# Performance work log

Measured on AMD Instinct MI355X. Metric: run time of the kernel, lower is better.

## Reference

```python
import jax, jax.numpy as jnp
import numpy as np

N = 100000      # nodes
E = 1600000     # edges
F_IN = 128      # num_features
H = 64          # hidden_channels
EPS = 1e-5      # batchnorm eps


def _bn(x, gamma, beta, mean, var):
    # inference-mode BatchNorm1d
    return (x - mean) * jax.lax.rsqrt(var + EPS) * gamma + beta


def setup_inputs() -> dict:
    key = jax.random.key(0)
    ks = jax.random.split(key, 16)

    def lin_w(k, fan_in, fan_out):
        return (jax.random.normal(k, (fan_in, fan_out), jnp.float32)
                * (1.0 / np.sqrt(fan_in)))

    return {
        "x": jax.random.normal(ks[0], (N, F_IN), jnp.float32),
        "edge_index": jax.random.randint(ks[1], (2, E), 0, N, dtype=jnp.int32),
        # node_encoder: Linear(F_IN,H) + BN
        "enc_W": lin_w(ks[2], F_IN, H), "enc_b": jnp.zeros((H,), jnp.float32),
        "enc_g": jnp.ones((H,), jnp.float32), "enc_beta": jnp.zeros((H,), jnp.float32),
        "enc_mean": jnp.zeros((H,), jnp.float32), "enc_var": jnp.ones((H,), jnp.float32),
        # GCNConv layers (PyG: lin without bias, bias added after aggregation)
        "conv1_W": lin_w(ks[3], H, H), "conv1_b": jnp.zeros((H,), jnp.float32),
        "conv2_W": lin_w(ks[4], H, H), "conv2_b": jnp.zeros((H,), jnp.float32),
        # edge_predictor: Linear(2H,H) + BN + Linear(H,1)
        "ep1_W": lin_w(ks[5], 2 * H, H), "ep1_b": jnp.zeros((H,), jnp.float32),
        "ep_g": jnp.ones((H,), jnp.float32), "ep_beta": jnp.zeros((H,), jnp.float32),
        "ep_mean": jnp.zeros((H,), jnp.float32), "ep_var": jnp.ones((H,), jnp.float32),
        "ep2_W": lin_w(ks[6], H, 1), "ep2_b": jnp.zeros((1,), jnp.float32),
    }


def reference(x, edge_index, enc_W, enc_b, enc_g, enc_beta, enc_mean, enc_var,
              conv1_W, conv1_b, conv2_W, conv2_b,
              ep1_W, ep1_b, ep_g, ep_beta, ep_mean, ep_var, ep2_W, ep2_b):
    row, col = edge_index[0], edge_index[1]

    # GCN normalization with added self-loops (symmetric D^-1/2 (A+I) D^-1/2)
    loops = jnp.arange(N, dtype=row.dtype)
    row_sl = jnp.concatenate([row, loops])          # [E+N]
    col_sl = jnp.concatenate([col, loops])
    deg = jax.ops.segment_sum(jnp.ones_like(col_sl, jnp.float32), col_sl, N)
    dinv = jnp.where(deg > 0, jax.lax.rsqrt(jnp.maximum(deg, 1.0)), 0.0)
    norm = dinv[row_sl] * dinv[col_sl]              # [E+N]

    def gcn_conv(h, W, b):
        hw = h @ W                                   # [N,H]
        msg = hw[row_sl] * norm[:, None]             # gather-scale  [E+N,H]
        return jax.ops.segment_sum(msg, col_sl, N) + b  # scatter-add

    # node encoder (inference: dropout = identity)
    h = jax.nn.relu(_bn(x @ enc_W + enc_b, enc_g, enc_beta, enc_mean, enc_var))
    h = jax.nn.relu(gcn_conv(h, conv1_W, conv1_b))
    h = jax.nn.relu(gcn_conv(h, conv2_W, conv2_b))
    node_embeddings = h

    # edge predictor: gather + cat + MLP + sigmoid
    ef = jnp.concatenate([h[row], h[col]], axis=1)   # [E, 2H]
    e = jax.nn.relu(_bn(ef @ ep1_W + ep1_b, ep_g, ep_beta, ep_mean, ep_var))
    edge_pred = jax.nn.sigmoid(e @ ep2_W + ep2_b)    # [E, 1]
    return node_embeddings, edge_pred
```

## Files before the change

### kernel.cpp

```cpp
#include <hip/hip_runtime.h>
#include <hip/hip_bf16.h>
#include <hip/hip_fp16.h>

#define NN 100000
#define NE 1600000
#define FIN 128
#define HD 64
#define NB_SCAN 391
#define NB_MF 1563
#define BSH 8
#define BUCK 256
#define NBUCK 392
#define BCAP 5120
#define CHUNK 4096
#define NCHUNK 391
#define ESPLIT 2
#define NEB (NBUCK*ESPLIT)
#define NFB 6250
#define NAGG 6250

typedef unsigned int uint32;
typedef _Float16 half8 __attribute__((ext_vector_type(8)));
typedef float f32x4 __attribute__((ext_vector_type(4)));
typedef float f32x8 __attribute__((ext_vector_type(8)));

__global__ void __launch_bounds__(256) k_part(const int* __restrict__ row,
                                              const int* __restrict__ col,
                                              int* __restrict__ bcnt,
                                              uint32* __restrict__ staged,
                                              uint32* __restrict__ posE){
    __shared__ int hist[NBUCK];
    __shared__ int base[NBUCK];
    int t = threadIdx.x;
    int e0 = blockIdx.x * CHUNK;
    int e1 = min(e0 + CHUNK, NE);
    for(int i = t; i < NBUCK; i += 256) hist[i] = 0;
    __syncthreads();
    for(int e = e0 + t; e < e1; e += 256)
        atomicAdd(&hist[col[e] >> BSH], 1);
    __syncthreads();
    for(int i = t; i < NBUCK; i += 256){
        int c = hist[i];
        base[i] = (c > 0) ? atomicAdd(&bcnt[i], c) : 0;
        hist[i] = 0;
    }
    __syncthreads();
    for(int e = e0 + t; e < e1; e += 256){
        int c = col[e], r = row[e];
        int b = c >> BSH;
        int pos = base[b] + atomicAdd(&hist[b], 1);
        if(pos < BCAP){
            staged[(size_t)b*BCAP + pos] = ((uint32)r << BSH) | (uint32)(c & (BUCK-1));
            posE[e] = (uint32)(b*BCAP + pos);
        } else posE[e] = 0xFFFFFFFFu;
    }
}

__global__ void __launch_bounds__(256) k_hist(const int* __restrict__ bcnt,
                                              const uint32* __restrict__ staged,
                                              int* __restrict__ deg){
    __shared__ int h[BUCK];
    int b = blockIdx.x, t = threadIdx.x;
    for(int i = t; i < BUCK; i += 256) h[i] = 0;
    __syncthreads();
    int cnt = min(bcnt[b], BCAP);
    const uint32* st = staged + (size_t)b*BCAP;
    for(int i = t; i < cnt; i += 256) atomicAdd(&h[st[i] & (BUCK-1)], 1);
    __syncthreads();
    for(int i = t; i < BUCK; i += 256){
        int n = b*BUCK + i;
        if(n < NN) deg[n] = h[i];
    }
}

__global__ void k_bsum(const int* __restrict__ deg, int* __restrict__ bsum){
    __shared__ int r[256];
    int t = threadIdx.x; int i = blockIdx.x*256 + t;
    r[t] = (i < NN) ? deg[i] : 0;
    __syncthreads();
    for(int off=128; off>0; off>>=1){ if(t<off) r[t]+=r[t+off]; __syncthreads(); }
    if(t==0) bsum[blockIdx.x] = r[0];
}

__global__ void k_top(int* __restrict__ bsum){
    __shared__ int s[512];
    int t = threadIdx.x;
    int v = (t < NB_SCAN) ? bsum[t] : 0;
    s[t] = v; __syncthreads();
    for(int off=1; off<512; off<<=1){
        int a = (t>=off)? s[t-off] : 0;
        __syncthreads();
        s[t] += a;
        __syncthreads();
    }
    if(t < NB_SCAN) bsum[t] = s[t] - v;
}

__global__ void k_scan(const int* __restrict__ deg, const int* __restrict__ bsum,
                       int* __restrict__ starts, float* __restrict__ dinv){
    __shared__ int s[256];
    int t = threadIdx.x; int i = blockIdx.x*256 + t;
    int d = (i<NN)? deg[i] : 0;
    s[t] = d; __syncthreads();
    for(int off=1; off<256; off<<=1){
        int a = (t>=off)? s[t-off] : 0;
        __syncthreads();
        s[t] += a;
        __syncthreads();
    }
    if(i < NN){
        starts[i] = bsum[blockIdx.x] + s[t] - d;
        dinv[i] = rsqrtf((float)(d + 1));
    }
}

__global__ void __launch_bounds__(256) k_fill2(const int* __restrict__ bcnt,
                                               const uint32* __restrict__ staged,
                                               const int* __restrict__ starts,
                                               int* __restrict__ csr){
    __shared__ int cur[BUCK];
    __shared__ int lcsr[BCAP];
    int b = blockIdx.x, t = threadIdx.x;
    int n0 = b*BUCK;
    int base = starts[min(n0, NN-1)];
    for(int i = t; i < BUCK; i += 256){
        int n = n0 + i;
        cur[i] = (n < NN) ? starts[n] - base : 0;
    }
    __syncthreads();
    int cnt = min(bcnt[b], BCAP);
    const uint32* st = staged + (size_t)b*BCAP;
    for(int i = t; i < cnt; i += 256){
        uint32 u = st[i];
        int p = atomicAdd(&cur[u & (BUCK-1)], 1);
        lcsr[p] = (int)(u >> BSH);
    }
    __syncthreads();
    for(int i = t; i < cnt; i += 256) csr[base + i] = lcsr[i];
}

__global__ void k_const(const float* __restrict__ encB, const float* __restrict__ encG,
                        const float* __restrict__ encBe, const float* __restrict__ encM,
                        const float* __restrict__ encV,
                        const float* __restrict__ ep1b, const float* __restrict__ epG,
                        const float* __restrict__ epBe, const float* __restrict__ epM,
                        const float* __restrict__ epV,
                        float* __restrict__ foldEnc, float* __restrict__ foldPre){
    int j = threadIdx.x;
    if(j < 64){
        float s = encG[j]*rsqrtf(encV[j]+1e-5f);
        foldEnc[j]      = s;
        foldEnc[64+j]   = (encB[j]-encM[j])*s + encBe[j];
        float sp = epG[j]*rsqrtf(epV[j]+1e-5f);
        foldPre[j]      = sp;
        foldPre[64+j]   = sp;
        foldPre[128+j]  = sp*(ep1b[j]-epM[j]) + epBe[j];
        foldPre[192+j]  = 0.f;
    }
}

__global__ void k_wprep(const float* __restrict__ encW, const float* __restrict__ c1W,
                        const float* __restrict__ c2W, const float* __restrict__ ep1W,
                        _Float16* __restrict__ wt){
    int i = blockIdx.x*256 + threadIdx.x;
    if(i < 8192){
        int n = i >> 7, k = i & 127;
        wt[i] = (_Float16)encW[k*64 + n];
    } else if(i < 12288){
        int j = i - 8192; int n = j >> 6, k = j & 63;
        wt[i] = (_Float16)c1W[k*64 + n];
    } else if(i < 16384){
        int j = i - 12288; int n = j >> 6, k = j & 63;
        wt[i] = (_Float16)c2W[k*64 + n];
    } else if(i < 24576){
        int j = i - 16384; int h = j >> 12; int jj = j & 4095;
        int n = jj >> 6, k = jj & 63;
        wt[i] = (_Float16)ep1W[(h*64 + k)*64 + n];
    }
}

template<int K, bool AF32, bool FOLD, bool RELU, bool SCALE, int OS>
__global__ void __launch_bounds__(256) k_mfma(const void* __restrict__ Ain,
                                              const _Float16* __restrict__ Bt,
                                              const float* __restrict__ fold,
                                              const float* __restrict__ rowscale,
                                              _Float16* __restrict__ outh){
    constexpr int PS = K + 8;
    __shared__ _Float16 As[64*PS];
    __shared__ _Float16 Bs[64*PS];
    int t = threadIdx.x;
    int m0 = blockIdx.x*64;
    int jh = blockIdx.y;
    {
        const _Float16* src = Bt + (size_t)jh*64*K;
        for(int idx = t; idx < 64*(K/8); idx += 256){
            int n = idx/(K/8), c = idx%(K/8);
            *(half8*)&Bs[n*PS + c*8] = *(const half8*)&src[n*K + c*8];
        }
    }
    if(AF32){
        const float* A = (const float*)Ain;
        for(int idx = t; idx < 64*(K/4); idx += 256){
            int r = idx/(K/4), c = idx%(K/4);
            int rowi = m0 + r; if(rowi >= NN) rowi = NN-1;
            float4 v = *(const float4*)&A[(size_t)rowi*K + c*4];
            _Float16* d = &As[r*PS + c*4];
            d[0]=(_Float16)v.x; d[1]=(_Float16)v.y; d[2]=(_Float16)v.z; d[3]=(_Float16)v.w;
        }
    } else {
        const _Float16* A = (const _Float16*)Ain;
        for(int idx = t; idx < 64*(K/8); idx += 256){
            int r = idx/(K/8), c = idx%(K/8);
            int rowi = m0 + r; if(rowi >= NN) rowi = NN-1;
            *(half8*)&As[r*PS + c*8] = *(const half8*)&A[(size_t)rowi*K + c*8];
        }
    }
    __syncthreads();
    int w = t>>6, l = t&63;
    int lm = l&15, q = l>>4;
    f32x4 acc0 = {0.f,0.f,0.f,0.f}, acc1 = {0.f,0.f,0.f,0.f};
    f32x4 acc2 = {0.f,0.f,0.f,0.f}, acc3 = {0.f,0.f,0.f,0.f};
    const _Float16* arow = &As[(w*16+lm)*PS + q*8];
    const _Float16* brow = &Bs[lm*PS + q*8];
    #pragma unroll
    for(int ks = 0; ks < K/32; ks++){
        half8 a  = *(const half8*)(arow + ks*32);
        half8 b0 = *(const half8*)(brow + ks*32);
        half8 b1 = *(const half8*)(brow + 16*PS + ks*32);
        half8 b2 = *(const half8*)(brow + 32*PS + ks*32);
        half8 b3 = *(const half8*)(brow + 48*PS + ks*32);
        acc0 = __builtin_amdgcn_mfma_f32_16x16x32_f16(a, b0, acc0, 0,0,0);
        acc1 = __builtin_amdgcn_mfma_f32_16x16x32_f16(a, b1, acc1, 0,0,0);
        acc2 = __builtin_amdgcn_mfma_f32_16x16x32_f16(a, b2, acc2, 0,0,0);
        acc3 = __builtin_amdgcn_mfma_f32_16x16x32_f16(a, b3, acc3, 0,0,0);
    }
    f32x4 accs[4] = {acc0, acc1, acc2, acc3};
    #pragma unroll
    for(int nt = 0; nt < 4; nt++){
        int col = nt*16 + lm;
        int jcol = jh*64 + col;
        float fs = FOLD ? fold[jcol] : 0.f;
        float fb = FOLD ? fold[OS + jcol] : 0.f;
        #pragma unroll
        for(int r = 0; r < 4; r++){
            int rowi = m0 + w*16 + q*4 + r;
            if(rowi >= NN) continue;
            float v = accs[nt][r];
            if(FOLD) v = v*fs + fb;
            if(RELU) v = fmaxf(v, 0.f);
            if(SCALE) v *= rowscale[rowi];
            outh[(size_t)rowi*OS + jcol] = (_Float16)v;
        }
    }
}

__global__ void __launch_bounds__(256) k_agg4(const _Float16* __restrict__ hb,
                                              const int* __restrict__ starts,
                                              const int* __restrict__ deg,
                                              const int* __restrict__ csr,
                                              const float* __restrict__ dinv,
                                              const float* __restrict__ bias,
                                              _Float16* __restrict__ outh,
                                              float* __restrict__ outf){
    int t = threadIdx.x, w = t>>6, f = t&63;
    int n0 = blockIdx.x*16 + w*4;
    int s0 = __builtin_amdgcn_readfirstlane(starts[n0+0]);
    int s1 = __builtin_amdgcn_readfirstlane(starts[n0+1]);
    int s2 = __builtin_amdgcn_readfirstlane(starts[n0+2]);
    int s3 = __builtin_amdgcn_readfirstlane(starts[n0+3]);
    int d0 = __builtin_amdgcn_readfirstlane(deg[n0+0]);
    int d1 = __builtin_amdgcn_readfirstlane(deg[n0+1]);
    int d2 = __builtin_amdgcn_readfirstlane(deg[n0+2]);
    int d3 = __builtin_amdgcn_readfirstlane(deg[n0+3]);
    float a0 = 0.f, a1 = 0.f, a2 = 0.f, a3 = 0.f;
    int dmax = max(max(d0,d1), max(d2,d3));
    for(int i0 = 0; i0 < dmax; i0 += 64){
        int li0 = (i0+f < d0) ? csr[s0+i0+f] : NN;
        int li1 = (i0+f < d1) ? csr[s1+i0+f] : NN;
        int li2 = (i0+f < d2) ? csr[s2+i0+f] : NN;
        int li3 = (i0+f < d3) ? csr[s3+i0+f] : NN;
        int mm = min(dmax - i0, 64);
        for(int j = 0; j < mm; j += 8){
            float t0 = 0.f, t1 = 0.f, t2 = 0.f, t3 = 0.f;
            #pragma unroll
            for(int u = 0; u < 8; u++){
                int r0 = __builtin_amdgcn_readlane(li0, j+u);
                int r1 = __builtin_amdgcn_readlane(li1, j+u);
                int r2 = __builtin_amdgcn_readlane(li2, j+u);
                int r3 = __builtin_amdgcn_readlane(li3, j+u);
                t0 += (float)hb[(size_t)r0*64 + f];
                t1 += (float)hb[(size_t)r1*64 + f];
                t2 += (float)hb[(size_t)r2*64 + f];
                t3 += (float)hb[(size_t)r3*64 + f];
            }
            a0 += t0; a1 += t1; a2 += t2; a3 += t3;
        }
    }
    float bv = bias[f];
    float dn0 = dinv[n0+0], dn1 = dinv[n0+1], dn2 = dinv[n0+2], dn3 = dinv[n0+3];
    float sf0 = (float)hb[(size_t)(n0+0)*64 + f];
    float sf1 = (float)hb[(size_t)(n0+1)*64 + f];
    float sf2 = (float)hb[(size_t)(n0+2)*64 + f];
    float sf3 = (float)hb[(size_t)(n0+3)*64 + f];
    float o0 = fmaxf((a0 + sf0)*dn0 + bv, 0.f);
    float o1 = fmaxf((a1 + sf1)*dn1 + bv, 0.f);
    float o2 = fmaxf((a2 + sf2)*dn2 + bv, 0.f);
    float o3 = fmaxf((a3 + sf3)*dn3 + bv, 0.f);
    outh[(size_t)(n0+0)*64 + f] = (_Float16)o0;
    outh[(size_t)(n0+1)*64 + f] = (_Float16)o1;
    outh[(size_t)(n0+2)*64 + f] = (_Float16)o2;
    outh[(size_t)(n0+3)*64 + f] = (_Float16)o3;
    if(outf){
        outf[(size_t)(n0+0)*64 + f] = o0;
        outf[(size_t)(n0+1)*64 + f] = o1;
        outf[(size_t)(n0+2)*64 + f] = o2;
        outf[(size_t)(n0+3)*64 + f] = o3;
    }
}

__global__ void __launch_bounds__(512) k_edgeb(const int* __restrict__ bcnt,
                                               const uint32* __restrict__ staged,
                                               const _Float16* __restrict__ pre,
                                               const float* __restrict__ w2,
                                               const float* __restrict__ b2,
                                               _Float16* __restrict__ zqh){
    __shared__ half8 Bl[BUCK*8];
    int t = threadIdx.x;
    int item = ((int)blockIdx.x & 7)*98 + ((int)blockIdx.x >> 3);
    int b = item >> 1, s = item & 1;
    const _Float16* ps = pre;
    for(int idx = t; idx < BUCK*8; idx += 512){
        int rl = idx >> 3, ch = idx & 7;
        int n = (b << BSH) + rl; if(n >= NN) n = NN-1;
        Bl[rl*8 + (ch ^ (rl & 7))] = *(const half8*)(ps + (size_t)n*128 + 64 + ch*8);
    }
    __syncthreads();

    int cnt = min(bcnt[b], BCAP);
    int lo = (cnt * s) >> 1, hi = (cnt * (s+1)) >> 1;
    const uint32* st = staged + (size_t)b*BCAP;
    _Float16* zb = zqh + (size_t)b*BCAP;
    int p  = t & 7;
    int oc = t >> 3;
    f32x8 w2v = *(const f32x8*)(w2 + 8*p);
    float b2v = b2[0];

    auto edot = [&](uint32 u)->float{
        int r  = (int)(u >> BSH);
        int cl = (int)(u & (BUCK-1));
        half8 av = *(const half8*)(ps + (size_t)r*128 + 8*p);
        half8 bv = Bl[cl*8 + (p ^ (cl & 7))];
        half8 sv = av + bv;
        half8 zero8 = {};
        half8 rv = __builtin_elementwise_max(sv, zero8);
        f32x8 fv = __builtin_convertvector(rv, f32x8);
        float z;
        z  = fv[0]*w2v[0] + fv[1]*w2v[1];
        z  = fmaf(fv[2], w2v[2], z); z = fmaf(fv[3], w2v[3], z);
        z  = fmaf(fv[4], w2v[4], z); z = fmaf(fv[5], w2v[5], z);
        z  = fmaf(fv[6], w2v[6], z); z = fmaf(fv[7], w2v[7], z);
        return z;
    };

    int i = lo + oc;
    for(; i + 64 < hi; i += 128){
        uint32 u0 = st[i], u1 = st[i+64];
        float z0 = edot(u0);
        float z1 = edot(u1);
        z0 += __shfl_xor(z0, 1, 64); z1 += __shfl_xor(z1, 1, 64);
        z0 += __shfl_xor(z0, 2, 64); z1 += __shfl_xor(z1, 2, 64);
        z0 += __shfl_xor(z0, 4, 64); z1 += __shfl_xor(z1, 4, 64);
        if(p == 0){
            zb[i]    = (_Float16)(1.f/(1.f+__expf(-(z0+b2v))));
            zb[i+64] = (_Float16)(1.f/(1.f+__expf(-(z1+b2v))));
        }
    }
    for(; i < hi; i += 64){
        uint32 u0 = st[i];
        float z0 = edot(u0);
        z0 += __shfl_xor(z0, 1, 64);
        z0 += __shfl_xor(z0, 2, 64);
        z0 += __shfl_xor(z0, 4, 64);
        if(p == 0) zb[i] = (_Float16)(1.f/(1.f+__expf(-(z0+b2v))));
    }
}

__global__ void __launch_bounds__(256) k_final(const uint32* __restrict__ posE,
                                               const _Float16* __restrict__ zqh,
                                               float* __restrict__ out){
    int e = blockIdx.x*256 + threadIdx.x;
    if(e < NE){
        uint32 pz = posE[e];
        out[e] = (float)zqh[pz < (uint32)(NBUCK*BCAP) ? pz : 0u];
    }
}


extern "C" void kernel_launch(void* const* d_in, const int* in_sizes, int n_in,
                              void* d_out, int out_size, void* d_ws, size_t ws_size,
                              hipStream_t stream){
    const float* x   = (const float*)d_in[0];
    const int* ei    = (const int*)d_in[1];
    const int* row   = ei;
    const int* col   = ei + NE;
    const float* encW = (const float*)d_in[2],  *encB = (const float*)d_in[3];
    const float* encG = (const float*)d_in[4],  *encBe= (const float*)d_in[5];
    const float* encM = (const float*)d_in[6],  *encV = (const float*)d_in[7];
    const float* c1W  = (const float*)d_in[8],  *c1b  = (const float*)d_in[9];
    const float* c2W  = (const float*)d_in[10], *c2b  = (const float*)d_in[11];
    const float* ep1W = (const float*)d_in[12], *ep1b = (const float*)d_in[13];
    const float* epG  = (const float*)d_in[14], *epBe = (const float*)d_in[15];
    const float* epM  = (const float*)d_in[16], *epV  = (const float*)d_in[17];
    const float* ep2W = (const float*)d_in[18], *ep2b = (const float*)d_in[19];

    char* wsc = (char*)d_ws;
    size_t o = 0;
    auto alloc = [&](size_t bytes)->void*{
        void* p = wsc + o; o += (bytes + 255) & ~(size_t)255; return p;
    };
    int*      deg     = (int*)     alloc((size_t)NN*4);
    int*      starts  = (int*)     alloc((size_t)NN*4);
    int*      bsum    = (int*)     alloc(1024*4);
    int*      bcnt    = (int*)     alloc((size_t)NBUCK*4);
    int*      csr     = (int*)     alloc((size_t)NE*4);
    uint32*   staged  = (uint32*)  alloc((size_t)NBUCK*BCAP*4);
    float*    dinv    = (float*)   alloc((size_t)NN*4);
    float*    foldEnc = (float*)   alloc(128*4);
    float*    foldPre = (float*)   alloc(256*4);
    _Float16* wt      = (_Float16*)alloc(24576*2);
    _Float16* bufA    = (_Float16*)alloc((size_t)NN*64*2);
    _Float16* bufB    = (_Float16*)alloc((size_t)(NN+1)*64*2);
    _Float16* preh    = (_Float16*)alloc((size_t)NN*128*2);
    uint32*   posE    = (uint32*)  alloc((size_t)NE*4);
    _Float16* zqh     = (_Float16*)alloc((size_t)NBUCK*BCAP*2);

    float* outp = (float*)d_out;
    float* node_out = outp;
    float* edge_out = outp + (size_t)NN*64;

    hipMemsetAsync(bcnt, 0, (size_t)NBUCK*4, stream);
    hipMemsetAsync(bufB + (size_t)NN*64, 0, 128, stream);
    k_part <<<NCHUNK,  256, 0, stream>>>(row, col, bcnt, staged, posE);
    k_hist <<<NBUCK,   256, 0, stream>>>(bcnt, staged, deg);
    k_bsum <<<NB_SCAN, 256, 0, stream>>>(deg, bsum);
    k_top  <<<1,       512, 0, stream>>>(bsum);
    k_scan <<<NB_SCAN, 256, 0, stream>>>(deg, bsum, starts, dinv);
    k_fill2<<<NBUCK,   256, 0, stream>>>(bcnt, staged, starts, csr);
    k_const<<<1, 64, 0, stream>>>(encB, encG, encBe, encM, encV,
                                  ep1b, epG, epBe, epM, epV, foldEnc, foldPre);
    k_wprep<<<96, 256, 0, stream>>>(encW, c1W, c2W, ep1W, wt);

    k_mfma<128,true,true,true,false,64><<<dim3(NB_MF,1), 256, 0, stream>>>
        (x, wt, foldEnc, nullptr, bufA);

    k_mfma<64,false,false,false,true,64><<<dim3(NB_MF,1), 256, 0, stream>>>
        (bufA, wt + 8192, nullptr, dinv, bufB);
    k_agg4 <<<NAGG, 256, 0, stream>>>(bufB, starts, deg, csr, dinv, c1b,
                                      bufA, nullptr);

    k_mfma<64,false,false,false,true,64><<<dim3(NB_MF,1), 256, 0, stream>>>
        (bufA, wt + 12288, nullptr, dinv, bufB);
    k_agg4 <<<NAGG, 256, 0, stream>>>(bufB, starts, deg, csr, dinv, c2b,
                                      bufA, node_out);

    k_mfma<64,false,true,false,false,128><<<dim3(NB_MF,2), 256, 0, stream>>>
        (bufA, wt + 16384, foldPre, nullptr, preh);

    k_edgeb<<<NEB, 512, 0, stream>>>(bcnt, staged, (const _Float16*)preh, ep2W, ep2b, zqh);
    k_final<<<NFB, 256, 0, stream>>>(posE, zqh, edge_out);
}
```

Before: 347.6 us.

## Fuse CSR build scan kernels and merge prep kernels to cut launches

Replaces the hist/bsum/top/scan/fill2 chain with a single k_fill3 kernel. Each bucket block computes its global base by summing the clamped counts of earlier buckets, then does a local scan to produce deg, starts, dinv and csr. The weight prep, BN folding and the two memsets move into one k_prep kernel. This cuts about seven launches and their serialization gaps, at the cost of each block redundantly reducing up to 392 counts.

```diff
diff --git a/kernel.cpp b/kernel.cpp
--- a/kernel.cpp
+++ b/kernel.cpp
@@ -6,7 +6,6 @@
 #define NE 1600000
 #define FIN 128
 #define HD 64
-#define NB_SCAN 391
 #define NB_MF 1563
 #define BSH 8
 #define BUCK 256
@@ -24,6 +23,51 @@
 typedef float f32x4 __attribute__((ext_vector_type(4)));
 typedef float f32x8 __attribute__((ext_vector_type(8)));
 
+__global__ void __launch_bounds__(256) k_prep(const float* __restrict__ encW, const float* __restrict__ c1W,
+                                              const float* __restrict__ c2W, const float* __restrict__ ep1W,
+                                              _Float16* __restrict__ wt,
+                                              const float* __restrict__ encB, const float* __restrict__ encG,
+                                              const float* __restrict__ encBe, const float* __restrict__ encM,
+                                              const float* __restrict__ encV,
+                                              const float* __restrict__ ep1b, const float* __restrict__ epG,
+                                              const float* __restrict__ epBe, const float* __restrict__ epM,
+                                              const float* __restrict__ epV,
+                                              float* __restrict__ foldEnc, float* __restrict__ foldPre,
+                                              int* __restrict__ bcnt, _Float16* __restrict__ bufBzero){
+    int blk = blockIdx.x, t = threadIdx.x;
+    if(blk < 96){
+        int i = blk*256 + t;
+        if(i < 8192){
+            int n = i >> 7, k = i & 127;
+            wt[i] = (_Float16)encW[k*64 + n];
+        } else if(i < 12288){
+            int j = i - 8192; int n = j >> 6, k = j & 63;
+            wt[i] = (_Float16)c1W[k*64 + n];
+        } else if(i < 16384){
+            int j = i - 12288; int n = j >> 6, k = j & 63;
+            wt[i] = (_Float16)c2W[k*64 + n];
+        } else {
+            int j = i - 16384; int h = j >> 12; int jj = j & 4095;
+            int n = jj >> 6, k = jj & 63;
+            wt[i] = (_Float16)ep1W[(h*64 + k)*64 + n];
+        }
+    } else {
+        if(t < 64){
+            int j = t;
+            float s = encG[j]*rsqrtf(encV[j]+1e-5f);
+            foldEnc[j]      = s;
+            foldEnc[64+j]   = (encB[j]-encM[j])*s + encBe[j];
+            float sp = epG[j]*rsqrtf(epV[j]+1e-5f);
+            foldPre[j]      = sp;
+            foldPre[64+j]   = sp;
+            foldPre[128+j]  = sp*(ep1b[j]-epM[j]) + epBe[j];
+            foldPre[192+j]  = 0.f;
+            bufBzero[j]     = (_Float16)0.f;
+        }
+        for(int i = t; i < NBUCK; i += 256) bcnt[i] = 0;
+    }
+}
+
 __global__ void __launch_bounds__(256) k_part(const int* __restrict__ row,
                                               const int* __restrict__ col,
                                               int* __restrict__ bcnt,
@@ -56,127 +100,55 @@
     }
 }
 
-__global__ void __launch_bounds__(256) k_hist(const int* __restrict__ bcnt,
-                                              const uint32* __restrict__ staged,
-                                              int* __restrict__ deg){
+__global__ void __launch_bounds__(256) k_fill3(const int* __restrict__ bcnt,
+                                               const uint32* __restrict__ staged,
+                                               int* __restrict__ deg,
+                                               int* __restrict__ starts,
+                                               float* __restrict__ dinv,
+                                               int* __restrict__ csr){
     __shared__ int h[BUCK];
+    __shared__ int sc[BUCK];
+    __shared__ int red[256];
+    __shared__ int lcsr[BCAP];
     int b = blockIdx.x, t = threadIdx.x;
-    for(int i = t; i < BUCK; i += 256) h[i] = 0;
+    int part = 0;
+    for(int i = t; i < b; i += 256) part += min(bcnt[i], BCAP);
+    red[t] = part; __syncthreads();
+    for(int off = 128; off > 0; off >>= 1){
+        if(t < off) red[t] += red[t+off];
+        __syncthreads();
+    }
+    int base = red[0];
+    h[t] = 0;
     __syncthreads();
     int cnt = min(bcnt[b], BCAP);
     const uint32* st = staged + (size_t)b*BCAP;
     for(int i = t; i < cnt; i += 256) atomicAdd(&h[st[i] & (BUCK-1)], 1);
     __syncthreads();
-    for(int i = t; i < BUCK; i += 256){
-        int n = b*BUCK + i;
-        if(n < NN) deg[n] = h[i];
-    }
-}
-
-__global__ void k_bsum(const int* __restrict__ deg, int* __restrict__ bsum){
-    __shared__ int r[256];
-    int t = threadIdx.x; int i = blockIdx.x*256 + t;
-    r[t] = (i < NN) ? deg[i] : 0;
-    __syncthreads();
-    for(int off=128; off>0; off>>=1){ if(t<off) r[t]+=r[t+off]; __syncthreads(); }
-    if(t==0) bsum[blockIdx.x] = r[0];
-}
-
-__global__ void k_top(int* __restrict__ bsum){
-    __shared__ int s[512];
-    int t = threadIdx.x;
-    int v = (t < NB_SCAN) ? bsum[t] : 0;
-    s[t] = v; __syncthreads();
-    for(int off=1; off<512; off<<=1){
-        int a = (t>=off)? s[t-off] : 0;
+    int v = h[t];
+    sc[t] = v; __syncthreads();
+    for(int off = 1; off < 256; off <<= 1){
+        int a = (t >= off) ? sc[t-off] : 0;
         __syncthreads();
-        s[t] += a;
+        sc[t] += a;
         __syncthreads();
     }
-    if(t < NB_SCAN) bsum[t] = s[t] - v;
-}
-
-__global__ void k_scan(const int* __restrict__ deg, const int* __restrict__ bsum,
-                       int* __restrict__ starts, float* __restrict__ dinv){
-    __shared__ int s[256];
-    int t = threadIdx.x; int i = blockIdx.x*256 + t;
-    int d = (i<NN)? deg[i] : 0;
-    s[t] = d; __syncthreads();
-    for(int off=1; off<256; off<<=1){
-        int a = (t>=off)? s[t-off] : 0;
-        __syncthreads();
-        s[t] += a;
-        __syncthreads();
-    }
-    if(i < NN){
-        starts[i] = bsum[blockIdx.x] + s[t] - d;
-        dinv[i] = rsqrtf((float)(d + 1));
-    }
-}
-
-__global__ void __launch_bounds__(256) k_fill2(const int* __restrict__ bcnt,
-                                               const uint32* __restrict__ staged,
-                                               const int* __restrict__ starts,
-                                               int* __restrict__ csr){
-    __shared__ int cur[BUCK];
-    __shared__ int lcsr[BCAP];
-    int b = blockIdx.x, t = threadIdx.x;
-    int n0 = b*BUCK;
-    int base = starts[min(n0, NN-1)];
-    for(int i = t; i < BUCK; i += 256){
-        int n = n0 + i;
-        cur[i] = (n < NN) ? starts[n] - base : 0;
-    }
-    __syncthreads();
-    int cnt = min(bcnt[b], BCAP);
-    const uint32* st = staged + (size_t)b*BCAP;
+    int ex = sc[t] - v;
+    int n = b*BUCK + t;
+    if(n < NN){
+        deg[n]    = v;
+        starts[n] = base + ex;
+        dinv[n]   = rsqrtf((float)(v + 1));
+    }
+    h[t] = ex;
+    __syncthreads();
     for(int i = t; i < cnt; i += 256){
         uint32 u = st[i];
-        int p = atomicAdd(&cur[u & (BUCK-1)], 1);
+        int p = atomicAdd(&h[u & (BUCK-1)], 1);
         lcsr[p] = (int)(u >> BSH);
     }
     __syncthreads();
     for(int i = t; i < cnt; i += 256) csr[base + i] = lcsr[i];
-}
-
-__global__ void k_const(const float* __restrict__ encB, const float* __restrict__ encG,
-                        const float* __restrict__ encBe, const float* __restrict__ encM,
-                        const float* __restrict__ encV,
-                        const float* __restrict__ ep1b, const float* __restrict__ epG,
-                        const float* __restrict__ epBe, const float* __restrict__ epM,
-                        const float* __restrict__ epV,
-                        float* __restrict__ foldEnc, float* __restrict__ foldPre){
-    int j = threadIdx.x;
-    if(j < 64){
-        float s = encG[j]*rsqrtf(encV[j]+1e-5f);
-        foldEnc[j]      = s;
-        foldEnc[64+j]   = (encB[j]-encM[j])*s + encBe[j];
-        float sp = epG[j]*rsqrtf(epV[j]+1e-5f);
-        foldPre[j]      = sp;
-        foldPre[64+j]   = sp;
-        foldPre[128+j]  = sp*(ep1b[j]-epM[j]) + epBe[j];
-        foldPre[192+j]  = 0.f;
-    }
-}
-
-__global__ void k_wprep(const float* __restrict__ encW, const float* __restrict__ c1W,
-                        const float* __restrict__ c2W, const float* __restrict__ ep1W,
-                        _Float16* __restrict__ wt){
-    int i = blockIdx.x*256 + threadIdx.x;
-    if(i < 8192){
-        int n = i >> 7, k = i & 127;
-        wt[i] = (_Float16)encW[k*64 + n];
-    } else if(i < 12288){
-        int j = i - 8192; int n = j >> 6, k = j & 63;
-        wt[i] = (_Float16)c1W[k*64 + n];
-    } else if(i < 16384){
-        int j = i - 12288; int n = j >> 6, k = j & 63;
-        wt[i] = (_Float16)c2W[k*64 + n];
-    } else if(i < 24576){
-        int j = i - 16384; int h = j >> 12; int jj = j & 4095;
-        int n = jj >> 6, k = jj & 63;
-        wt[i] = (_Float16)ep1W[(h*64 + k)*64 + n];
-    }
 }
 
 template<int K, bool AF32, bool FOLD, bool RELU, bool SCALE, int OS>
@@ -420,7 +392,6 @@
     };
     int*      deg     = (int*)     alloc((size_t)NN*4);
     int*      starts  = (int*)     alloc((size_t)NN*4);
-    int*      bsum    = (int*)     alloc(1024*4);
     int*      bcnt    = (int*)     alloc((size_t)NBUCK*4);
     int*      csr     = (int*)     alloc((size_t)NE*4);
     uint32*   staged  = (uint32*)  alloc((size_t)NBUCK*BCAP*4);
@@ -438,17 +409,12 @@
     float* node_out = outp;
     float* edge_out = outp + (size_t)NN*64;
 
-    hipMemsetAsync(bcnt, 0, (size_t)NBUCK*4, stream);
-    hipMemsetAsync(bufB + (size_t)NN*64, 0, 128, stream);
-    k_part <<<NCHUNK,  256, 0, stream>>>(row, col, bcnt, staged, posE);
-    k_hist <<<NBUCK,   256, 0, stream>>>(bcnt, staged, deg);
-    k_bsum <<<NB_SCAN, 256, 0, stream>>>(deg, bsum);
-    k_top  <<<1,       512, 0, stream>>>(bsum);
-    k_scan <<<NB_SCAN, 256, 0, stream>>>(deg, bsum, starts, dinv);
-    k_fill2<<<NBUCK,   256, 0, stream>>>(bcnt, staged, starts, csr);
-    k_const<<<1, 64, 0, stream>>>(encB, encG, encBe, encM, encV,
-                                  ep1b, epG, epBe, epM, epV, foldEnc, foldPre);
-    k_wprep<<<96, 256, 0, stream>>>(encW, c1W, c2W, ep1W, wt);
+    k_prep <<<97, 256, 0, stream>>>(encW, c1W, c2W, ep1W, wt,
+                                    encB, encG, encBe, encM, encV,
+                                    ep1b, epG, epBe, epM, epV,
+                                    foldEnc, foldPre, bcnt, bufB + (size_t)NN*64);
+    k_part <<<NCHUNK, 256, 0, stream>>>(row, col, bcnt, staged, posE);
+    k_fill3<<<NBUCK,  256, 0, stream>>>(bcnt, staged, deg, starts, dinv, csr);
 
     k_mfma<128,true,true,true,false,64><<<dim3(NB_MF,1), 256, 0, stream>>>
         (x, wt, foldEnc, nullptr, bufA);
```

Result: faster. 334.6 us (-3.7%).
